# Optimization experiments

Hardware: AMD Instinct MI355X
Metric: run time of the kernel (lower is better)

## Reference

```python
import jax, jax.numpy as jnp
import numpy as np

N = 100000
E = 1600000
D_IN = 128
D_OUT = 128
D_DEC = 2
TAU = 0.5
NEG_SLOPE = 0.2  # PyG GATv2Conv default negative_slope


def _glorot(key, shape):
    lim = (6.0 / (shape[0] + shape[1])) ** 0.5
    return jax.random.uniform(key, shape, jnp.float32, -lim, lim)


def gatv2(x, edge_index, Wl, Wr, bl, br, att, bias):
    """PyG GATv2Conv, heads=1, add_self_loops=True, eval mode (no dropout).
    out[i] = sum_j softmax_i( att . leaky_relu(xl[j] + xr[i]) ) * xl[j] + bias
    """
    n = x.shape[0]
    loops = jnp.arange(n, dtype=edge_index.dtype)
    src = jnp.concatenate([edge_index[0], loops])  # [E+N]
    dst = jnp.concatenate([edge_index[1], loops])
    xl = x @ Wl + bl  # [N, out]
    xr = x @ Wr + br
    # per-edge unnormalized score
    e = jax.nn.leaky_relu(xl[src] + xr[dst], NEG_SLOPE) @ att  # [E+N]
    # scatter-softmax over incoming edges of each target node
    m = jax.ops.segment_max(e, dst, num_segments=n)
    a = jnp.exp(e - m[dst])
    s = jax.ops.segment_sum(a, dst, num_segments=n)
    alpha = a / (s[dst] + 1e-16)
    out = jax.ops.segment_sum(alpha[:, None] * xl[src], dst, num_segments=n)
    return out + bias


def setup_inputs() -> dict:
    key = jax.random.key(0)
    ks = jax.random.split(key, 16)
    x = jax.random.normal(ks[0], (N, D_IN), jnp.float32)
    edge_dec = jax.random.randint(ks[1], (2, E), 0, N, jnp.int64)
    edge_0 = jax.random.randint(ks[2], (2, E), 0, N, jnp.int64)
    edge_1 = jax.random.randint(ks[3], (2, E), 0, N, jnp.int64)
    u = jax.random.uniform(ks[4], (N, D_DEC), jnp.float32, 1e-6, 1.0 - 1e-6)
    gumbel = -jnp.log(-jnp.log(u))  # Gumbel(0,1) noise
    # shared GAT (used for every decision branch)
    Wl_g = _glorot(ks[5], (D_IN, D_OUT))
    Wr_g = _glorot(ks[6], (D_IN, D_OUT))
    bl_g = jnp.zeros((D_OUT,), jnp.float32)
    br_g = jnp.zeros((D_OUT,), jnp.float32)
    att_g = _glorot(ks[7], (D_OUT, 1))[:, 0]
    bias_g = jnp.zeros((D_OUT,), jnp.float32)
    # decision GAT
    Wl_d = _glorot(ks[8], (D_IN, D_DEC))
    Wr_d = _glorot(ks[9], (D_IN, D_DEC))
    bl_d = jnp.zeros((D_DEC,), jnp.float32)
    br_d = jnp.zeros((D_DEC,), jnp.float32)
    att_d = _glorot(ks[10], (D_DEC, 1))[:, 0]
    bias_d = jnp.zeros((D_DEC,), jnp.float32)
    return {"x": x, "edge_dec": edge_dec, "edge_0": edge_0, "edge_1": edge_1,
            "gumbel": gumbel,
            "Wl_g": Wl_g, "Wr_g": Wr_g, "bl_g": bl_g, "br_g": br_g,
            "att_g": att_g, "bias_g": bias_g,
            "Wl_d": Wl_d, "Wr_d": Wr_d, "bl_d": bl_d, "br_d": br_d,
            "att_d": att_d, "bias_d": bias_d}


def reference(x, edge_dec, edge_0, edge_1, gumbel,
              Wl_g, Wr_g, bl_g, br_g, att_g, bias_g,
              Wl_d, Wr_d, bl_d, br_d, att_d, bias_d):
    # decision logits via decision GAT on the decision edge set
    logits = gatv2(x, edge_dec, Wl_d, Wr_d, bl_d, br_d, att_d, bias_d)  # [N, 2]
    # hard gumbel-softmax with straight-through estimator, tau=0.5
    y_soft = jax.nn.softmax((logits + gumbel) / TAU, axis=-1)
    idx = jnp.argmax(y_soft, axis=-1)
    y_hard = jax.nn.one_hot(idx, y_soft.shape[-1], dtype=y_soft.dtype)
    decisions = y_hard + y_soft - jax.lax.stop_gradient(y_soft)
    # per-decision GAT (shared weights, different edge sets), gated sum
    out = jnp.zeros((x.shape[0], Wl_g.shape[1]), x.dtype)
    for i, ei in enumerate([edge_0, edge_1]):
        out = out + gatv2(x, ei, Wl_g, Wr_g, bl_g, br_g, att_g, bias_g) * decisions[:, i:i + 1]
    return out
```

## Files before the change

kernel.cpp:

```cpp
#include <hip/hip_runtime.h>

#define NEG 0.2f
#define CAPD16 384
#define CAPC16 704
#define CH 9216
#define NT 512
#define CSH 9
#define FPC 32
#define NSL 4
#define NCMAX 256
#define CHB 512
#define CCAPD 9216
#define CCAPC 17408
#define FIT 9

typedef __attribute__((ext_vector_type(8))) short short8;
typedef __attribute__((ext_vector_type(4))) float f32x4;

static __device__ __forceinline__ unsigned short f2bf(float f) {
  unsigned u = __float_as_uint(f);
  u += 0x7fffu + ((u >> 16) & 1u);
  return (unsigned short)(u >> 16);
}
static __device__ __forceinline__ float bflo(unsigned u) {
  return __uint_as_float(u << 16);
}
static __device__ __forceinline__ float bfhi(unsigned u) {
  return __uint_as_float(u & 0xffff0000u);
}
static __device__ __forceinline__ float bfx(const uint4& v, int f) {
  unsigned c = (f < 2) ? v.x : (f < 4) ? v.y : (f < 6) ? v.z : v.w;
  return (f & 1) ? bfhi(c) : bflo(c);
}
static __device__ __forceinline__ unsigned f2u(float f) {
  unsigned b = __float_as_uint(f);
  return (b & 0x80000000u) ? ~b : (b | 0x80000000u);
}
static __device__ __forceinline__ float u2f(unsigned u) {
  unsigned b = (u & 0x80000000u) ? (u ^ 0x80000000u) : ~u;
  return __uint_as_float(b);
}

__global__ void k_prep_wt(const float* __restrict__ Wl, const float* __restrict__ Wr,
                          unsigned short* __restrict__ wt, int* __restrict__ zbuf,
                          int ncur) {
  if (blockIdx.x < 128) {
    int idx = blockIdx.x * 256 + threadIdx.x;
    int c = idx >> 7, k = idx & 127;
    float v = (c < 128) ? Wl[(size_t)k * 128 + c] : Wr[(size_t)k * 128 + (c - 128)];
    wt[idx] = f2bf(v);
  } else {
    int i = (blockIdx.x - 128) * 256 + threadIdx.x;
    if (i < ncur) zbuf[i] = 0;
  }
}

__global__ __launch_bounds__(256) void k_gemm_main(
    const float* __restrict__ x, const unsigned short* __restrict__ wt,
    const float* __restrict__ bl, const float* __restrict__ br,
    const float* __restrict__ Wld, const float* __restrict__ Wrd,
    const float* __restrict__ bld, const float* __restrict__ brd,
    unsigned short* __restrict__ xl, unsigned short* __restrict__ xr,
    float* __restrict__ xld, float* __restrict__ xrd, int N) {
  __shared__ unsigned short sx[32][272];
  int w = threadIdx.x >> 6, lane = threadIdx.x & 63;
  int m = lane & 15, quad = lane >> 4;
  int rowbase = blockIdx.x * 32;
  if (rowbase >= N) return;
  int colbase = w * 64;
  f32x4 acc0[4] = {}, acc1[4] = {};
  float dl0 = 0.f, dl1 = 0.f, dr0 = 0.f, dr1 = 0.f;
  int rc0 = rowbase + m;      if (rc0 >= N) rc0 = N - 1;
  int rc1 = rowbase + 16 + m; if (rc1 >= N) rc1 = N - 1;
  const float* arow0 = x + (size_t)rc0 * 128 + quad * 8;
  const float* arow1 = x + (size_t)rc1 * 128 + quad * 8;
#pragma unroll
  for (int kb = 0; kb < 128; kb += 32) {
    float4 a00 = *(const float4*)(arow0 + kb);
    float4 a01 = *(const float4*)(arow0 + kb + 4);
    float4 a10 = *(const float4*)(arow1 + kb);
    float4 a11 = *(const float4*)(arow1 + kb + 4);
    if (w < 2) {
      float4 A = (w == 0) ? a00 : a10;
      float4 B = (w == 0) ? a01 : a11;
      int k0 = kb + quad * 8;
      const float4* wl4 = (const float4*)(Wld + 2 * k0);
      const float4* wr4 = (const float4*)(Wrd + 2 * k0);
      float4 l0 = wl4[0], l1 = wl4[1], l2 = wl4[2], l3 = wl4[3];
      float4 r0 = wr4[0], r1 = wr4[1], r2 = wr4[2], r3 = wr4[3];
      dl0 = fmaf(A.x, l0.x, dl0); dl1 = fmaf(A.x, l0.y, dl1);
      dl0 = fmaf(A.y, l0.z, dl0); dl1 = fmaf(A.y, l0.w, dl1);
      dl0 = fmaf(A.z, l1.x, dl0); dl1 = fmaf(A.z, l1.y, dl1);
      dl0 = fmaf(A.w, l1.z, dl0); dl1 = fmaf(A.w, l1.w, dl1);
      dl0 = fmaf(B.x, l2.x, dl0); dl1 = fmaf(B.x, l2.y, dl1);
      dl0 = fmaf(B.y, l2.z, dl0); dl1 = fmaf(B.y, l2.w, dl1);
      dl0 = fmaf(B.z, l3.x, dl0); dl1 = fmaf(B.z, l3.y, dl1);
      dl0 = fmaf(B.w, l3.z, dl0); dl1 = fmaf(B.w, l3.w, dl1);
      dr0 = fmaf(A.x, r0.x, dr0); dr1 = fmaf(A.x, r0.y, dr1);
      dr0 = fmaf(A.y, r0.z, dr0); dr1 = fmaf(A.y, r0.w, dr1);
      dr0 = fmaf(A.z, r1.x, dr0); dr1 = fmaf(A.z, r1.y, dr1);
      dr0 = fmaf(A.w, r1.z, dr0); dr1 = fmaf(A.w, r1.w, dr1);
      dr0 = fmaf(B.x, r2.x, dr0); dr1 = fmaf(B.x, r2.y, dr1);
      dr0 = fmaf(B.y, r2.z, dr0); dr1 = fmaf(B.y, r2.w, dr1);
      dr0 = fmaf(B.z, r3.x, dr0); dr1 = fmaf(B.z, r3.y, dr1);
      dr0 = fmaf(B.w, r3.z, dr0); dr1 = fmaf(B.w, r3.w, dr1);
    }
    short8 af0, af1;
    af0[0] = (short)f2bf(a00.x); af0[1] = (short)f2bf(a00.y);
    af0[2] = (short)f2bf(a00.z); af0[3] = (short)f2bf(a00.w);
    af0[4] = (short)f2bf(a01.x); af0[5] = (short)f2bf(a01.y);
    af0[6] = (short)f2bf(a01.z); af0[7] = (short)f2bf(a01.w);
    af1[0] = (short)f2bf(a10.x); af1[1] = (short)f2bf(a10.y);
    af1[2] = (short)f2bf(a10.z); af1[3] = (short)f2bf(a10.w);
    af1[4] = (short)f2bf(a11.x); af1[5] = (short)f2bf(a11.y);
    af1[6] = (short)f2bf(a11.z); af1[7] = (short)f2bf(a11.w);
#pragma unroll
    for (int ct = 0; ct < 4; ct++) {
      const unsigned short* bp =
          wt + (size_t)(colbase + ct * 16 + m) * 128 + kb + quad * 8;
      short8 bfr = *(const short8*)bp;
      acc0[ct] = __builtin_amdgcn_mfma_f32_16x16x32_bf16(af0, bfr, acc0[ct], 0, 0, 0);
      acc1[ct] = __builtin_amdgcn_mfma_f32_16x16x32_bf16(af1, bfr, acc1[ct], 0, 0, 0);
    }
  }
  if (w < 2) {
    dl0 += __shfl_xor(dl0, 16); dl0 += __shfl_xor(dl0, 32);
    dl1 += __shfl_xor(dl1, 16); dl1 += __shfl_xor(dl1, 32);
    dr0 += __shfl_xor(dr0, 16); dr0 += __shfl_xor(dr0, 32);
    dr1 += __shfl_xor(dr1, 16); dr1 += __shfl_xor(dr1, 32);
    if (quad == 0) {
      int row = rowbase + w * 16 + m;
      if (row < N) {
        float2 vl; vl.x = dl0 + bld[0]; vl.y = dl1 + bld[1];
        float2 vr; vr.x = dr0 + brd[0]; vr.y = dr1 + brd[1];
        *(float2*)(xld + 2 * (size_t)row) = vl;
        *(float2*)(xrd + 2 * (size_t)row) = vr;
      }
    }
  }
#pragma unroll
  for (int ct = 0; ct < 4; ct++) {
    int c = colbase + ct * 16 + m;
    float badd = (c < 128) ? bl[c] : br[c - 128];
#pragma unroll
    for (int r = 0; r < 4; r++) {
      sx[quad * 4 + r][c]      = f2bf(acc0[ct][r] + badd);
      sx[16 + quad * 4 + r][c] = f2bf(acc1[ct][r] + badd);
    }
  }
  __syncthreads();
  {
    int row = threadIdx.x >> 3, chunk = threadIdx.x & 7;
    int gr = rowbase + row;
    if (gr < N) {
      const uint4* src = (const uint4*)&sx[row][chunk * 32];
      uint4* dst = (chunk < 4)
          ? (uint4*)(xl + (size_t)gr * 128 + chunk * 32)
          : (uint4*)(xr + (size_t)gr * 128 + (chunk - 4) * 32);
      dst[0] = src[0]; dst[1] = src[1]; dst[2] = src[2]; dst[3] = src[3];
    }
  }
}

__global__ __launch_bounds__(NT) void k_bin_coarse(
    const int* __restrict__ ed, const int* __restrict__ e0,
    const int* __restrict__ e1, int* __restrict__ gccur,
    unsigned* __restrict__ cbind, unsigned* __restrict__ cbinc,
    long E, int NC) {
  __shared__ unsigned stage[CH];
  __shared__ int h[CHB + 1];
  __shared__ int gbase[CHB];
  __shared__ int wtot[8], wexcl[8];
  int tid = threadIdx.x;
  long base = (long)blockIdx.x * CH;
  long T = 3 * E;
  for (int a = tid; a < CHB + 1; a += NT) h[a] = 0;
  __syncthreads();
  unsigned pays[CH / NT];
  int has[CH / NT];
#pragma unroll
  for (int it = 0; it < CH / NT; it++) {
    long idx = base + it * NT + tid;
    int ha = -1; unsigned pay = 0;
    if (idx < T) {
      if (idx < E) {
        int s = ed[idx], t = ed[E + idx];
        ha = t >> CSH;
        pay = ((unsigned)s << CSH) | (unsigned)(t & ((1 << CSH) - 1));
      } else {
        int k = idx >= 2 * E;
        const int* L = k ? e1 : e0;
        long j = idx - E - (k ? E : 0);
        int s = L[j], t = L[E + j];
        ha = NCMAX + (t >> CSH);
        pay = ((unsigned)s << (CSH + 1)) | ((unsigned)k << CSH) |
              (unsigned)(t & ((1 << CSH) - 1));
      }
      atomicAdd(&h[ha], 1);
    }
    pays[it] = pay; has[it] = ha;
  }
  __syncthreads();
  {
    int v = h[tid];
    int lane = tid & 63, wv = tid >> 6;
    int inc = v;
    for (int off = 1; off < 64; off <<= 1) {
      int nv = __shfl_up(inc, off);
      if (lane >= off) inc += nv;
    }
    if (lane == 63) wtot[wv] = inc;
    __syncthreads();
    if (tid == 0) {
      int r = 0;
      for (int i = 0; i < 8; i++) { wexcl[i] = r; r += wtot[i]; }
    }
    __syncthreads();
    int excl = wexcl[wv] + inc - v;
    h[tid] = excl;
    if (tid == NT - 1) h[CHB] = excl + v;
  }
  __syncthreads();
  {
    int a = tid;
    int cnt = h[a + 1] - h[a];
    if (cnt > 0) {
      if (a < NCMAX) { if (a < NC) gbase[a] = atomicAdd(&gccur[a], cnt); }
      else { int b = a - NCMAX; if (b < NC) gbase[a] = atomicAdd(&gccur[NC + b], cnt); }
    }
  }
  __syncthreads();
#pragma unroll
  for (int it = 0; it < CH / NT; it++) {
    int ha = has[it];
    if (ha >= 0) {
      int pos = atomicAdd(&h[ha], 1);
      stage[pos] = pays[it];
    }
  }
  __syncthreads();
  int lane = tid & 63, wv = tid >> 6;
  for (int a = wv; a < 2 * NCMAX; a += 8) {
    int start = a ? h[a - 1] : 0;
    int end = h[a];
    int len = end - start;
    if (len <= 0) continue;
    int gb = gbase[a];
    if (a < NCMAX) {
      if (a < NC) {
        unsigned* dst = cbind + (size_t)a * CCAPD;
        for (int i = lane; i < len; i += 64) {
          int o = gb + i;
          if (o < CCAPD) dst[o] = stage[start + i];
        }
      }
    } else {
      int b = a - NCMAX;
      if (b < NC) {
        unsigned* dst = cbinc + (size_t)b * CCAPC;
        for (int i = lane; i < len; i += 64) {
          int o = gb + i;
          if (o < CCAPC) dst[o] = stage[start + i];
        }
      }
    }
  }
}

__global__ __launch_bounds__(NT) void k_bin_fine(
    const unsigned* __restrict__ cbind, const unsigned* __restrict__ cbinc,
    const int* __restrict__ gccur, unsigned* __restrict__ bind,
    unsigned* __restrict__ binc, int* __restrict__ cntd, int* __restrict__ cntc,
    int NC, int NB16) {
  __shared__ int hh[FPC];
  __shared__ int gb[FPC];
  int blk = blockIdx.x;
  int cb = blk >> 2, sl = blk & (NSL - 1);
  int isC = cb >= NC;
  int c = isC ? cb - NC : cb;
  int cnt = gccur[cb];
  int ccap = isC ? CCAPC : CCAPD;
  if (cnt > ccap) cnt = ccap;
  int ssz = (cnt + NSL - 1) / NSL;
  int s0 = sl * ssz;
  int s1 = s0 + ssz; if (s1 > cnt) s1 = cnt;
  const unsigned* src = isC ? (cbinc + (size_t)c * CCAPC)
                            : (cbind + (size_t)c * CCAPD);
  int tid = threadIdx.x;
  if (tid < FPC) hh[tid] = 0;
  __syncthreads();
  unsigned pays[FIT]; int fs[FIT];
#pragma unroll
  for (int it = 0; it < FIT; it++) {
    int i = s0 + it * NT + tid;
    int f = -1; unsigned pay = 0;
    if (i < s1) {
      pay = src[i];
      f = (pay >> 4) & (FPC - 1);
      atomicAdd(&hh[f], 1);
    }
    pays[it] = pay; fs[it] = f;
  }
  __syncthreads();
  if (tid < FPC) {
    int v = hh[tid];
    int base = 0;
    int fb = c * FPC + tid;
    if (v > 0 && fb < NB16)
      base = atomicAdd(isC ? &cntc[fb] : &cntd[fb], v);
    gb[tid] = base;
    hh[tid] = 0;
  }
  __syncthreads();
#pragma unroll
  for (int it = 0; it < FIT; it++) {
    int f = fs[it];
    if (f >= 0) {
      unsigned pay = pays[it];
      int fb = c * FPC + f;
      int pos = gb[f] + atomicAdd(&hh[f], 1);
      if (isC) {
        unsigned o = ((pay >> (CSH + 1)) << 5) | (((pay >> CSH) & 1u) << 4) |
                     (pay & 15u);
        if (pos < CAPC16 && fb < NB16) binc[(size_t)fb * CAPC16 + pos] = o;
      } else {
        unsigned o = ((pay >> CSH) << 4) | (pay & 15u);
        if (pos < CAPD16 && fb < NB16) bind[(size_t)fb * CAPD16 + pos] = o;
      }
    }
  }
}

__global__ __launch_bounds__(256) void k_fused(
    const unsigned* __restrict__ bind, const unsigned* __restrict__ binc,
    const int* __restrict__ cntd_, const int* __restrict__ cntc_,
    const unsigned short* __restrict__ xl, const unsigned short* __restrict__ xr,
    const float* __restrict__ xld, const float* __restrict__ xrd,
    const float* __restrict__ attd, const float* __restrict__ biasd,
    const float* __restrict__ g, const float* __restrict__ att,
    const float* __restrict__ bias, float* __restrict__ out, int N) {
  __shared__ float xrd_s[32];
  __shared__ unsigned nmax[16];
  __shared__ float nsum[16], na0[16], na1[16];
  __shared__ int dec_s[16], scnt[16];
  __shared__ int slots[16 * 65];
  int tid = threadIdx.x;
  int b = blockIdx.x, nb0 = b << 4;
  int cdn = cntd_[b]; if (cdn > CAPD16) cdn = CAPD16;
  int ccn = cntc_[b]; if (ccn > CAPC16) ccn = CAPC16;
  float a0 = attd[0], a1 = attd[1];
  float eself = 0.f, x0s = 0.f, x1s = 0.f;
  if (tid < 16) {
    int node = nb0 + tid;
    if (node < N) {
      float2 xrv = *(const float2*)(xrd + 2 * (size_t)node);
      xrd_s[2 * tid] = xrv.x; xrd_s[2 * tid + 1] = xrv.y;
      float2 xlv = *(const float2*)(xld + 2 * (size_t)node);
      x0s = xlv.x; x1s = xlv.y;
      float h0 = x0s + xrv.x, h1 = x1s + xrv.y;
      eself = a0 * fmaxf(h0, NEG * h0) + a1 * fmaxf(h1, NEG * h1);
      nmax[tid] = f2u(eself);
    } else {
      xrd_s[2 * tid] = 0.f; xrd_s[2 * tid + 1] = 0.f;
      nmax[tid] = f2u(0.f);
    }
    nsum[tid] = 0.f; na0[tid] = 0.f; na1[tid] = 0.f;
  }
  __syncthreads();
  const unsigned* bd = bind + (size_t)b * CAPD16;
  const float2* xld2 = (const float2*)xld;
  auto dscore = [&](float2 v, int tl) {
    float h0 = v.x + xrd_s[2 * tl], h1 = v.y + xrd_s[2 * tl + 1];
    return a0 * fmaxf(h0, NEG * h0) + a1 * fmaxf(h1, NEG * h1);
  };
  unsigned pkA = 0, pkB = 0;
  float2 vA, vB; vA.x = vA.y = vB.x = vB.y = 0.f;
  float sA = 0.f, sB = 0.f;
  bool okA = tid < cdn, okB = tid + 256 < cdn;
  if (okA) {
    pkA = bd[tid]; vA = xld2[pkA >> 4];
    sA = dscore(vA, pkA & 15);
    atomicMax(&nmax[pkA & 15], f2u(sA));
  }
  if (okB) {
    pkB = bd[tid + 256]; vB = xld2[pkB >> 4];
    sB = dscore(vB, pkB & 15);
    atomicMax(&nmax[pkB & 15], f2u(sB));
  }
  __syncthreads();
  if (okA) {
    int tl = pkA & 15;
    float w = expf(sA - u2f(nmax[tl]));
    atomicAdd(&nsum[tl], w); atomicAdd(&na0[tl], w * vA.x); atomicAdd(&na1[tl], w * vA.y);
  }
  if (okB) {
    int tl = pkB & 15;
    float w = expf(sB - u2f(nmax[tl]));
    atomicAdd(&nsum[tl], w); atomicAdd(&na0[tl], w * vB.x); atomicAdd(&na1[tl], w * vB.y);
  }
  __syncthreads();
  if (tid < 16) {
    int node = nb0 + tid;
    if (node < N) {
      float mm = u2f(nmax[tid]);
      float ws = expf(eself - mm);
      float den = nsum[tid] + ws + 1e-16f;
      float z0 = (na0[tid] + ws * x0s) / den + biasd[0] + g[2 * (size_t)node];
      float z1 = (na1[tid] + ws * x1s) / den + biasd[1] + g[2 * (size_t)node + 1];
      dec_s[tid] = (z1 > z0) ? 1 : 0;
      scnt[tid] = 1; slots[tid * 65] = node;
    } else {
      dec_s[tid] = -1; scnt[tid] = 0; slots[tid * 65] = 0;
    }
  }
  __syncthreads();
  const unsigned* bc = binc + (size_t)b * CAPC16;
  for (int i = tid; i < ccn; i += 256) {
    unsigned pk = bc[i];
    int tl = pk & 15, k = (pk >> 4) & 1;
    if (k == dec_s[tl]) {
      int pos = atomicAdd(&scnt[tl], 1);
      if (pos < 64) slots[tl * 65 + pos] = pk >> 5;
    }
  }
  __syncthreads();

  int l = tid & 15, gg = tid >> 4;
  const float4* at4 = (const float4*)att;
  float4 atA = at4[l * 2], atB = at4[l * 2 + 1];
  float a6[8] = {0.6f * atA.x, 0.6f * atA.y, 0.6f * atA.z, 0.6f * atA.w,
                 0.6f * atB.x, 0.6f * atB.y, 0.6f * atB.z, 0.6f * atB.w};
  float a4[8] = {0.4f * atA.x, 0.4f * atA.y, 0.4f * atA.z, 0.4f * atA.w,
                 0.4f * atB.x, 0.4f * atB.y, 0.4f * atB.z, 0.4f * atB.w};

  int nd = nb0 + gg;
  bool nvalid = nd < N;
  int cnt = scnt[gg]; if (cnt > 64) cnt = 64;
  if (!nvalid) cnt = 0;
  int mc = max(cnt, __shfl_xor(cnt, 16));
  mc = max(mc, __shfl_xor(mc, 32));

  int nc = nvalid ? nd : 0;
  uint4 xrp = ((const uint4*)(xr + (size_t)nc * 128))[l];
  float xrv[8] = {bflo(xrp.x), bfhi(xrp.x), bflo(xrp.y), bfhi(xrp.y),
                  bflo(xrp.z), bfhi(xrp.z), bflo(xrp.w), bfhi(xrp.w)};

  int cl = cnt - 1; if (cl < 0) cl = 0;
  const int* srow = &slots[gg * 65];
  uint4 cur[8];
#pragma unroll
  for (int j = 0; j < 8; j++) {
    int idx = j > cl ? cl : j;
    cur[j] = ((const uint4*)(xl + (size_t)srow[idx] * 128))[l];
  }
  float m = -3.0e38f, lsum = 0.f;
  float gacc[8] = {0.f, 0.f, 0.f, 0.f, 0.f, 0.f, 0.f, 0.f};

  for (int e = 0; e < mc; e += 8) {
    uint4 nxt[8];
#pragma unroll
    for (int j = 0; j < 8; j++) {
      int idx = e + 8 + j; if (idx > cl) idx = cl;
      nxt[j] = ((const uint4*)(xl + (size_t)srow[idx] * 128))[l];
    }
    float p[8];
#pragma unroll
    for (int j = 0; j < 8; j++) {
      float pa = 0.f, pb = 0.f;
#pragma unroll
      for (int f = 0; f < 8; f++) {
        float h = bfx(cur[j], f) + xrv[f];
        pa = fmaf(a6[f], h, pa);
        pb = fmaf(a4[f], fabsf(h), pb);
      }
      p[j] = pa + pb;
    }
#pragma unroll
    for (int off = 1; off < 16; off <<= 1) {
#pragma unroll
      for (int j = 0; j < 8; j++) p[j] += __shfl_xor(p[j], off);
    }
#pragma unroll
    for (int j = 0; j < 8; j++) p[j] = (e + j < cnt) ? p[j] : -3.0e38f;
    float nm = m;
#pragma unroll
    for (int j = 0; j < 8; j++) nm = fmaxf(nm, p[j]);
    float sc = __expf(m - nm);
    lsum *= sc;
#pragma unroll
    for (int f = 0; f < 8; f++) gacc[f] *= sc;
#pragma unroll
    for (int j = 0; j < 8; j++) {
      float w = __expf(p[j] - nm);
      lsum += w;
#pragma unroll
      for (int f = 0; f < 8; f++) gacc[f] = fmaf(w, bfx(cur[j], f), gacc[f]);
    }
    m = nm;
#pragma unroll
    for (int j = 0; j < 8; j++) cur[j] = nxt[j];
  }
  if (nvalid) {
    const float4* b4 = (const float4*)bias;
    float4 bA = b4[l * 2], bB = b4[l * 2 + 1];
    float inv = 1.0f / (lsum + 1e-16f);
    float4 oA, oB;
    oA.x = gacc[0] * inv + bA.x; oA.y = gacc[1] * inv + bA.y;
    oA.z = gacc[2] * inv + bA.z; oA.w = gacc[3] * inv + bA.w;
    oB.x = gacc[4] * inv + bB.x; oB.y = gacc[5] * inv + bB.y;
    oB.z = gacc[6] * inv + bB.z; oB.w = gacc[7] * inv + bB.w;
    float4* op = (float4*)(out + (size_t)nd * 128 + l * 8);
    op[0] = oA; op[1] = oB;
  }
}

extern "C" void kernel_launch(void* const* d_in, const int* in_sizes, int n_in,
                              void* d_out, int out_size, void* d_ws, size_t ws_size,
                              hipStream_t stream) {
  const float* x      = (const float*)d_in[0];
  const int*   ed     = (const int*)d_in[1];
  const int*   e0     = (const int*)d_in[2];
  const int*   e1     = (const int*)d_in[3];
  const float* gumbel = (const float*)d_in[4];
  const float* Wl_g   = (const float*)d_in[5];
  const float* Wr_g   = (const float*)d_in[6];
  const float* bl_g   = (const float*)d_in[7];
  const float* br_g   = (const float*)d_in[8];
  const float* att_g  = (const float*)d_in[9];
  const float* bias_g = (const float*)d_in[10];
  const float* Wl_d   = (const float*)d_in[11];
  const float* Wr_d   = (const float*)d_in[12];
  const float* bl_d   = (const float*)d_in[13];
  const float* br_d   = (const float*)d_in[14];
  const float* att_d  = (const float*)d_in[15];
  const float* bias_d = (const float*)d_in[16];

  const int  N    = in_sizes[0] / 128;
  const long E    = in_sizes[1] / 2;
  const int  NB16 = (N + 15) / 16;
  const int  NC   = (N + (1 << CSH) - 1) >> CSH;

  char* p = (char*)d_ws;
  auto alloc = [&](size_t bytes) -> void* {
    void* r = (void*)p;
    p += (bytes + 255) & ~(size_t)255;
    return r;
  };
  unsigned short* xl = (unsigned short*)alloc((size_t)N * 128 * 2);
  unsigned short* xr = (unsigned short*)alloc((size_t)N * 128 * 2);
  unsigned short* wt = (unsigned short*)alloc((size_t)256 * 128 * 2);
  float* xld      = (float*)alloc((size_t)N * 2 * 4);
  float* xrd      = (float*)alloc((size_t)N * 2 * 4);
  const int nz    = 2 * NC + 2 * NB16;
  int* zbuf       = (int*)alloc((size_t)nz * 4);
  unsigned* bind  = (unsigned*)alloc((size_t)NB16 * CAPD16 * 4);
  unsigned* binc  = (unsigned*)alloc((size_t)NB16 * CAPC16 * 4);
  int* gccur = zbuf;
  int* cntd  = zbuf + 2 * NC;
  int* cntc  = cntd + NB16;
  unsigned* cbind = (unsigned*)xl;
  unsigned* cbinc = (unsigned*)xr;

  const int gB = (int)((3 * E + CH - 1) / CH);
  const int gZ = (nz + 255) / 256;

  k_prep_wt<<<128 + gZ, 256, 0, stream>>>(Wl_g, Wr_g, wt, zbuf, nz);
  k_bin_coarse<<<gB, NT, 0, stream>>>(ed, e0, e1, gccur, cbind, cbinc, E, NC);
  k_bin_fine<<<2 * NC * NSL, NT, 0, stream>>>(cbind, cbinc, gccur, bind, binc,
                                              cntd, cntc, NC, NB16);
  k_gemm_main<<<(N + 31) / 32, 256, 0, stream>>>(x, wt, bl_g, br_g, Wl_d, Wr_d,
                                                 bl_d, br_d, xl, xr, xld, xrd, N);
  k_fused<<<NB16, 256, 0, stream>>>(bind, binc, cntd, cntc, xl, xr, xld, xrd,
                                    att_d, bias_d, gumbel, att_g, bias_g,
                                    (float*)d_out, N);
}
```

Before: 382.0 us.

## Fold weight prep into binning kernel, memset counters, and halve edge batch in fused GAT

Removes the separate weight-transpose/zeroing kernel. The bf16 weight conversion now runs in 64 extra blocks appended to the coarse binning launch, and the counters are cleared with hipMemsetAsync. In the fused attention kernel the per-node edge batch drops from 8 to 4 gathered rows, the softmax update is rewritten as explicit chained FMAs, and the bias load is hoisted. The aims are one fewer launch and lower register pressure for better occupancy, at the cost of less memory-level parallelism per thread in the gather loop.

```diff
diff --git a/kernel.cpp b/kernel.cpp
--- a/kernel.cpp
+++ b/kernel.cpp
@@ -39,20 +39,6 @@
 static __device__ __forceinline__ float u2f(unsigned u) {
   unsigned b = (u & 0x80000000u) ? (u ^ 0x80000000u) : ~u;
   return __uint_as_float(b);
-}
-
-__global__ void k_prep_wt(const float* __restrict__ Wl, const float* __restrict__ Wr,
-                          unsigned short* __restrict__ wt, int* __restrict__ zbuf,
-                          int ncur) {
-  if (blockIdx.x < 128) {
-    int idx = blockIdx.x * 256 + threadIdx.x;
-    int c = idx >> 7, k = idx & 127;
-    float v = (c < 128) ? Wl[(size_t)k * 128 + c] : Wr[(size_t)k * 128 + (c - 128)];
-    wt[idx] = f2bf(v);
-  } else {
-    int i = (blockIdx.x - 128) * 256 + threadIdx.x;
-    if (i < ncur) zbuf[i] = 0;
-  }
 }
 
 __global__ __launch_bounds__(256) void k_gemm_main(
@@ -166,7 +152,16 @@
     const int* __restrict__ ed, const int* __restrict__ e0,
     const int* __restrict__ e1, int* __restrict__ gccur,
     unsigned* __restrict__ cbind, unsigned* __restrict__ cbinc,
-    long E, int NC) {
+    const float* __restrict__ Wl, const float* __restrict__ Wr,
+    unsigned short* __restrict__ wt,
+    long E, int NC, int gB) {
+  if (blockIdx.x >= gB) {
+    int idx = (blockIdx.x - gB) * NT + threadIdx.x;
+    int c = idx >> 7, k = idx & 127;
+    float v = (c < 128) ? Wl[(size_t)k * 128 + c] : Wr[(size_t)k * 128 + (c - 128)];
+    wt[idx] = f2bf(v);
+    return;
+  }
   __shared__ unsigned stage[CH];
   __shared__ int h[CHB + 1];
   __shared__ int gbase[CHB];
@@ -432,6 +427,8 @@
                  0.6f * atB.x, 0.6f * atB.y, 0.6f * atB.z, 0.6f * atB.w};
   float a4[8] = {0.4f * atA.x, 0.4f * atA.y, 0.4f * atA.z, 0.4f * atA.w,
                  0.4f * atB.x, 0.4f * atB.y, 0.4f * atB.z, 0.4f * atB.w};
+  const float4* b4 = (const float4*)bias;
+  float4 bA = b4[l * 2], bB = b4[l * 2 + 1];
 
   int nd = nb0 + gg;
   bool nvalid = nd < N;
@@ -447,25 +444,25 @@
 
   int cl = cnt - 1; if (cl < 0) cl = 0;
   const int* srow = &slots[gg * 65];
-  uint4 cur[8];
-#pragma unroll
-  for (int j = 0; j < 8; j++) {
+  uint4 cur[4];
+#pragma unroll
+  for (int j = 0; j < 4; j++) {
     int idx = j > cl ? cl : j;
     cur[j] = ((const uint4*)(xl + (size_t)srow[idx] * 128))[l];
   }
   float m = -3.0e38f, lsum = 0.f;
   float gacc[8] = {0.f, 0.f, 0.f, 0.f, 0.f, 0.f, 0.f, 0.f};
 
-  for (int e = 0; e < mc; e += 8) {
-    uint4 nxt[8];
-#pragma unroll
-    for (int j = 0; j < 8; j++) {
-      int idx = e + 8 + j; if (idx > cl) idx = cl;
+  for (int e = 0; e < mc; e += 4) {
+    uint4 nxt[4];
+#pragma unroll
+    for (int j = 0; j < 4; j++) {
+      int idx = e + 4 + j; if (idx > cl) idx = cl;
       nxt[j] = ((const uint4*)(xl + (size_t)srow[idx] * 128))[l];
     }
-    float p[8];
-#pragma unroll
-    for (int j = 0; j < 8; j++) {
+    float p[4];
+#pragma unroll
+    for (int j = 0; j < 4; j++) {
       float pa = 0.f, pb = 0.f;
 #pragma unroll
       for (int f = 0; f < 8; f++) {
@@ -477,32 +474,30 @@
     }
 #pragma unroll
     for (int off = 1; off < 16; off <<= 1) {
-#pragma unroll
-      for (int j = 0; j < 8; j++) p[j] += __shfl_xor(p[j], off);
-    }
-#pragma unroll
-    for (int j = 0; j < 8; j++) p[j] = (e + j < cnt) ? p[j] : -3.0e38f;
-    float nm = m;
-#pragma unroll
-    for (int j = 0; j < 8; j++) nm = fmaxf(nm, p[j]);
+      p[0] += __shfl_xor(p[0], off); p[1] += __shfl_xor(p[1], off);
+      p[2] += __shfl_xor(p[2], off); p[3] += __shfl_xor(p[3], off);
+    }
+    float pe0 = (e     < cnt) ? p[0] : -3.0e38f;
+    float pe1 = (e + 1 < cnt) ? p[1] : -3.0e38f;
+    float pe2 = (e + 2 < cnt) ? p[2] : -3.0e38f;
+    float pe3 = (e + 3 < cnt) ? p[3] : -3.0e38f;
+    float nm = fmaxf(m, fmaxf(fmaxf(pe0, pe1), fmaxf(pe2, pe3)));
     float sc = __expf(m - nm);
-    lsum *= sc;
-#pragma unroll
-    for (int f = 0; f < 8; f++) gacc[f] *= sc;
-#pragma unroll
-    for (int j = 0; j < 8; j++) {
-      float w = __expf(p[j] - nm);
-      lsum += w;
-#pragma unroll
-      for (int f = 0; f < 8; f++) gacc[f] = fmaf(w, bfx(cur[j], f), gacc[f]);
+    float w0 = __expf(pe0 - nm), w1 = __expf(pe1 - nm);
+    float w2 = __expf(pe2 - nm), w3 = __expf(pe3 - nm);
+    lsum = lsum * sc + w0 + w1 + w2 + w3;
+#pragma unroll
+    for (int f = 0; f < 8; f++) {
+      float t0 = fmaf(w0, bfx(cur[0], f), gacc[f] * sc);
+      float t1 = fmaf(w1, bfx(cur[1], f), t0);
+      float t2 = fmaf(w2, bfx(cur[2], f), t1);
+      gacc[f]  = fmaf(w3, bfx(cur[3], f), t2);
     }
     m = nm;
 #pragma unroll
-    for (int j = 0; j < 8; j++) cur[j] = nxt[j];
+    for (int j = 0; j < 4; j++) cur[j] = nxt[j];
   }
   if (nvalid) {
-    const float4* b4 = (const float4*)bias;
-    float4 bA = b4[l * 2], bB = b4[l * 2 + 1];
     float inv = 1.0f / (lsum + 1e-16f);
     float4 oA, oB;
     oA.x = gacc[0] * inv + bA.x; oA.y = gacc[1] * inv + bA.y;
@@ -562,10 +557,10 @@
   unsigned* cbinc = (unsigned*)xr;
 
   const int gB = (int)((3 * E + CH - 1) / CH);
-  const int gZ = (nz + 255) / 256;
-
-  k_prep_wt<<<128 + gZ, 256, 0, stream>>>(Wl_g, Wr_g, wt, zbuf, nz);
-  k_bin_coarse<<<gB, NT, 0, stream>>>(ed, e0, e1, gccur, cbind, cbinc, E, NC);
+
+  hipMemsetAsync(zbuf, 0, (size_t)nz * 4, stream);
+  k_bin_coarse<<<gB + 64, NT, 0, stream>>>(ed, e0, e1, gccur, cbind, cbinc,
+                                           Wl_g, Wr_g, wt, E, NC, gB);
   k_bin_fine<<<2 * NC * NSL, NT, 0, stream>>>(cbind, cbinc, gccur, bind, binc,
                                               cntd, cntc, NC, NB16);
   k_gemm_main<<<(N + 31) / 32, 256, 0, stream>>>(x, wt, bl_g, br_g, Wl_d, Wr_d,
```

Result: faster. 367.8 us (median of 2 runs) (-3.7%).
